# Optimization experiments

Measured on AMD Instinct MI355X. Metric: run time of the kernel, lower is better.

## Reference

```python
import jax, jax.numpy as jnp
from jax import lax
import numpy as np

AE_THRESHOLD = 0.5


def setup_inputs() -> dict:
    key = jax.random.key(0)
    ks = jax.random.split(key, 8)
    B, C, H, W = 8, 80, 128, 128
    return {
        "tl_heat": jax.random.normal(ks[0], (B, C, H, W), jnp.float32),
        "br_heat": jax.random.normal(ks[1], (B, C, H, W), jnp.float32),
        "ct_heat": jax.random.normal(ks[2], (B, C, H, W), jnp.float32),
        "tl_tag": jax.random.normal(ks[3], (B, 1, H, W), jnp.float32),
        "br_tag": jax.random.normal(ks[4], (B, 1, H, W), jnp.float32),
        "tl_regr": jax.random.normal(ks[5], (B, 2, H, W), jnp.float32),
        "br_regr": jax.random.normal(ks[6], (B, 2, H, W), jnp.float32),
        "ct_regr": jax.random.normal(ks[7], (B, 2, H, W), jnp.float32),
        "K": 100,
        "kernel": 3,
        "num_dets": 1000,
    }


def _nms(heat, kernel):
    # maxpool NMS: keep only local maxima (SAME padding, stride 1, NCHW)
    hmax = lax.reduce_window(heat, -jnp.inf, lax.max,
                             (1, 1, kernel, kernel), (1, 1, 1, 1), 'SAME')
    return heat * (hmax == heat).astype(heat.dtype)


def _topk(scores, K):
    B, C, H, W = scores.shape
    s, inds = lax.top_k(scores.reshape(B, -1), K)  # over cat*H*W
    clses = inds // (H * W)
    inds = inds % (H * W)
    ys = (inds // W).astype(jnp.float32)
    xs = (inds % W).astype(jnp.float32)
    return s, inds, clses, ys, xs


def _gather(feat, inds):
    # NCHW -> (B, H*W, C), gather spatial rows by inds (B, K) -> (B, K, C)
    B, C, H, W = feat.shape
    f = feat.transpose(0, 2, 3, 1).reshape(B, H * W, C)
    return jnp.take_along_axis(f, inds[:, :, None], axis=1)


def reference(tl_heat, br_heat, ct_heat, tl_tag, br_tag,
              tl_regr, br_regr, ct_regr, K, kernel, num_dets):
    B, C, H, W = tl_heat.shape

    tl_heat = _nms(jax.nn.sigmoid(tl_heat), kernel)
    br_heat = _nms(jax.nn.sigmoid(br_heat), kernel)
    ct_heat = _nms(jax.nn.sigmoid(ct_heat), kernel)

    tl_s, tl_inds, tl_clses, tl_ys, tl_xs = _topk(tl_heat, K)
    br_s, br_inds, br_clses, br_ys, br_xs = _topk(br_heat, K)
    ct_s, ct_inds, ct_clses, ct_ys, ct_xs = _topk(ct_heat, K)

    tl_off = _gather(tl_regr, tl_inds)  # (B, K, 2)
    br_off = _gather(br_regr, br_inds)
    ct_off = _gather(ct_regr, ct_inds)

    # corner coords with sub-pixel offsets; broadcast to (B, K, K) pairs
    tl_xs_p = (tl_xs + tl_off[..., 0])[:, :, None]  # (B, K, 1)
    tl_ys_p = (tl_ys + tl_off[..., 1])[:, :, None]
    br_xs_p = (br_xs + br_off[..., 0])[:, None, :]  # (B, 1, K)
    br_ys_p = (br_ys + br_off[..., 1])[:, None, :]
    ct_xs_p = ct_xs + ct_off[..., 0]                # (B, K)
    ct_ys_p = ct_ys + ct_off[..., 1]

    pair = (B, K, K)
    bboxes = jnp.stack([jnp.broadcast_to(tl_xs_p, pair),
                        jnp.broadcast_to(tl_ys_p, pair),
                        jnp.broadcast_to(br_xs_p, pair),
                        jnp.broadcast_to(br_ys_p, pair)], axis=-1)  # (B,K,K,4)

    tl_emb = _gather(tl_tag, tl_inds)[:, :, 0]  # (B, K)
    br_emb = _gather(br_tag, br_inds)[:, :, 0]
    dists = jnp.abs(tl_emb[:, :, None] - br_emb[:, None, :])  # (B,K,K)

    scores = (tl_s[:, :, None] + br_s[:, None, :]) * 0.5
    reject = ((tl_clses[:, :, None] != br_clses[:, None, :])
              | (dists > AE_THRESHOLD)
              | (br_xs_p < tl_xs_p)
              | (br_ys_p < tl_ys_p))
    scores = jnp.where(reject, -jnp.ones_like(scores), scores)

    scores, inds = lax.top_k(scores.reshape(B, -1), num_dets)  # (B, num_dets)

    bboxes = jnp.take_along_axis(bboxes.reshape(B, K * K, 4),
                                 inds[:, :, None], axis=1)
    clses_full = jnp.broadcast_to(tl_clses[:, :, None], pair).reshape(B, K * K)
    clses = jnp.take_along_axis(clses_full, inds, axis=1).astype(jnp.float32)
    tl_s_full = jnp.broadcast_to(tl_s[:, :, None], pair).reshape(B, K * K)
    br_s_full = jnp.broadcast_to(br_s[:, None, :], pair).reshape(B, K * K)
    tl_sc = jnp.take_along_axis(tl_s_full, inds, axis=1)
    br_sc = jnp.take_along_axis(br_s_full, inds, axis=1)

    detections = jnp.concatenate([bboxes, scores[..., None], tl_sc[..., None],
                                  br_sc[..., None], clses[..., None]], axis=-1)
    center = jnp.stack([ct_xs_p, ct_ys_p,
                        ct_clses.astype(jnp.float32), ct_s], axis=-1)  # (B,K,4)
    return detections, center
```

## Files before the change

### kernel.cpp

```cpp
#include <hip/hip_runtime.h>
#include <cstdint>

#define NB    8
#define NC    80
#define HH    128
#define WW    128
#define HW    16384
#define CHW   1310720
#define KTOP  100
#define NDET  1000
#define NPAIR 10000
#define CAP   4096
#define ACAP  2048
#define NBINS 4096
#define VTHR  3.5f

#define OFF_CCNT   0
#define OFF_CCNT2  3072
#define OFF_HIST   6144
#define ZERO_BYTES 399360
#define OFF_THR    399360
#define OFF_CAND   399488
#define OFF_CS     1185920
#define OFF_CX     1195520
#define OFF_CY     1205120
#define OFF_CE     1214720
#define OFF_CCLS   1224320
#define WS_NEEDED  1233920

__device__ __forceinline__ float sigmoidf(float x) {
    float e = expf(-fabsf(x));
    return (x >= 0.f ? 1.f : e) / (1.f + e);
}

__global__ void __launch_bounds__(512) k_nms(
        const float* __restrict__ tl, const float* __restrict__ br,
        const float* __restrict__ ct,
        uint64_t* __restrict__ cand, int* __restrict__ ccnt) {
    __shared__ float lds[HW];

    int tid = threadIdx.x;
    int bid = blockIdx.x;
    int bc = bid / NC;
    int chan = bid - bc * NC;
    int t = bc >> 3; int b = bc & 7;
    const float* heat = (t == 0) ? tl : (t == 1) ? br : ct;
    const float* cb = heat + (size_t)b * CHW + (size_t)chan * HW;
    int lane = tid & 63;
    int w = tid >> 6;

    #pragma unroll
    for (int it = 0; it < 8; ++it) {
        int fbase = (it * 8 + w) * 256;
        __builtin_amdgcn_global_load_lds(
            (const __attribute__((address_space(1))) void*)(cb + fbase + lane * 4),
            (__attribute__((address_space(3))) void*)(&lds[fbase]),
            16, 0, 0);
    }
    asm volatile("s_waitcnt vmcnt(0)" ::: "memory");
    __syncthreads();

    int tile_x = (tid & 31) * 4;
    int tile_y = (tid >> 5) * 8;
    const float NEG = -__builtin_inff();
    float4 A, B, C;
    if (tile_y > 0) A = *(const float4*)&lds[(tile_y - 1) * WW + tile_x];
    else            A = make_float4(NEG, NEG, NEG, NEG);
    B = *(const float4*)&lds[tile_y * WW + tile_x];

    int ccbase = bc * 32;
    uint64_t* cd = cand + (size_t)bc * CAP;
    int ibase = chan * HW + tile_y * WW + tile_x;

    #pragma unroll
    for (int j = 0; j < 8; ++j) {
        int yn = tile_y + j + 1;
        if (yn < HH) C = *(const float4*)&lds[yn * WW + tile_x];
        else         C = make_float4(NEG, NEG, NEG, NEG);

        float c0 = fmaxf(fmaxf(A.x, B.x), C.x);
        float c1 = fmaxf(fmaxf(A.y, B.y), C.y);
        float c2 = fmaxf(fmaxf(A.z, B.z), C.z);
        float c3 = fmaxf(fmaxf(A.w, B.w), C.w);
        float cl = __shfl_up(c3, 1);
        float cr = __shfl_down(c0, 1);
        if (tile_x == 0)      cl = NEG;
        if (tile_x == WW - 4) cr = NEG;
        float w0 = fmaxf(fmaxf(cl, c0), c1);
        float w1 = fmaxf(fmaxf(c0, c1), c2);
        float w2 = fmaxf(fmaxf(c1, c2), c3);
        float w3 = fmaxf(fmaxf(c2, c3), cr);

        #define EMIT(Wm, V, P) \
            if ((Wm) == (V) && (V) >= VTHR) { \
                uint32_t bt = __float_as_uint(sigmoidf(V)); \
                int pos = atomicAdd(&ccnt[ccbase], 1); \
                if (pos < CAP) \
                    cd[pos] = ((uint64_t)bt << 32) | \
                              (uint32_t)(~(uint32_t)(ibase + j * WW + (P))); \
            }
        EMIT(w0, B.x, 0)
        EMIT(w1, B.y, 1)
        EMIT(w2, B.z, 2)
        EMIT(w3, B.w, 3)
        #undef EMIT
        A = B; B = C;
    }
}

__device__ uint64_t key_at(const float* __restrict__ hb, int i) {
    float v = hb[i];
    int rem = i & (HW - 1);
    int y = rem >> 7, x = rem & (WW - 1);
    bool mx = true;
    if (y > 0) {
        if (x > 0      && hb[i - WW - 1] > v) mx = false;
        if (              hb[i - WW    ] > v) mx = false;
        if (x < WW - 1 && hb[i - WW + 1] > v) mx = false;
    }
    if (x > 0      && hb[i - 1] > v) mx = false;
    if (x < WW - 1 && hb[i + 1] > v) mx = false;
    if (y < HH - 1) {
        if (x > 0      && hb[i + WW - 1] > v) mx = false;
        if (              hb[i + WW    ] > v) mx = false;
        if (x < WW - 1 && hb[i + WW + 1] > v) mx = false;
    }
    if (!mx) return 0;
    return ((uint64_t)__float_as_uint(sigmoidf(v)) << 32) | (uint32_t)(~(uint32_t)i);
}

__device__ __forceinline__ bool fast_ok(const int* ccnt, int bc) {
    int n = ccnt[bc * 32];
    return (n >= KTOP) && (n <= CAP);
}

__global__ void __launch_bounds__(256) fb_hist(
        const int* __restrict__ ccnt,
        const float* __restrict__ tl, const float* __restrict__ br,
        const float* __restrict__ ct, uint32_t* __restrict__ hist) {
    int bc = blockIdx.y;
    if (fast_ok(ccnt, bc)) return;
    __shared__ uint32_t lh[NBINS];
    for (int i = threadIdx.x; i < NBINS; i += 256) lh[i] = 0;
    __syncthreads();
    int t = bc >> 3; int b = bc & 7;
    const float* heat = (t == 0) ? tl : (t == 1) ? br : ct;
    const float* hb = heat + (size_t)b * CHW;
    for (int i = blockIdx.x * 256 + threadIdx.x; i < CHW; i += 32 * 256) {
        uint64_t k = key_at(hb, i);
        if (k) atomicAdd(&lh[(uint32_t)(k >> 51)], 1u);
    }
    __syncthreads();
    uint32_t* gh = hist + (size_t)bc * NBINS;
    for (int i = threadIdx.x; i < NBINS; i += 256) {
        uint32_t c = lh[i];
        if (c) atomicAdd(&gh[i], c);
    }
}

__global__ void __launch_bounds__(256) fb_thresh(
        const int* __restrict__ ccnt, const uint32_t* __restrict__ hist,
        int* __restrict__ thr) {
    int bc = blockIdx.x;
    if (fast_ok(ccnt, bc)) return;
    __shared__ uint32_t csum[256];
    const uint32_t* h = hist + (size_t)bc * NBINS;
    int tid = threadIdx.x;
    uint32_t bins[16];
    #pragma unroll
    for (int i = 0; i < 16; ++i) bins[i] = h[tid * 16 + i];
    if (tid == 0) bins[0] = 0;
    uint32_t s = 0;
    #pragma unroll
    for (int i = 0; i < 16; ++i) s += bins[i];
    csum[tid] = s;
    __syncthreads();
    for (int step = 1; step < 256; step <<= 1) {
        uint32_t add = (tid + step < 256) ? csum[tid + step] : 0;
        __syncthreads();
        csum[tid] += add;
        __syncthreads();
    }
    uint32_t inc = csum[tid];
    uint32_t above = (tid + 1 < 256) ? csum[tid + 1] : 0;
    if (tid == 0 && inc < KTOP) thr[bc] = 1;
    if (above < KTOP && inc >= KTOP) {
        uint32_t cum = above;
        int T = 1;
        #pragma unroll
        for (int i = 15; i >= 0; --i) {
            cum += bins[i];
            if (cum >= KTOP) { T = tid * 16 + i; break; }
        }
        thr[bc] = T;
    }
}

__global__ void __launch_bounds__(256) fb_collect(
        const int* __restrict__ ccnt, const int* __restrict__ thr,
        const float* __restrict__ tl, const float* __restrict__ br,
        const float* __restrict__ ct,
        uint64_t* __restrict__ cand, int* __restrict__ ccnt2) {
    int bc = blockIdx.y;
    if (fast_ok(ccnt, bc)) return;
    int t = bc >> 3; int b = bc & 7;
    const float* heat = (t == 0) ? tl : (t == 1) ? br : ct;
    const float* hb = heat + (size_t)b * CHW;
    int T = thr[bc];
    for (int i = blockIdx.x * 256 + threadIdx.x; i < CHW; i += 32 * 256) {
        uint64_t k = key_at(hb, i);
        if (k && (int)(uint32_t)(k >> 51) >= T) {
            int pc = atomicAdd(&ccnt2[bc * 32], 1);
            if (pc < CAP) cand[(size_t)bc * CAP + pc] = k;
        }
    }
}

template <int N>
__device__ void bitonic_desc(uint64_t* k) {
    for (int kk = 2; kk <= N; kk <<= 1) {
        for (int j = kk >> 1; j > 0; j >>= 1) {
            __syncthreads();
            for (int i = threadIdx.x; i < N; i += blockDim.x) {
                int l = i ^ j;
                if (l > i) {
                    uint64_t a = k[i], b = k[l];
                    bool up = ((i & kk) == 0);
                    if (up ? (a < b) : (a > b)) { k[i] = b; k[l] = a; }
                }
            }
        }
    }
    __syncthreads();
}

__global__ void __launch_bounds__(1024) k_select(
        const uint64_t* __restrict__ cand, const int* __restrict__ ccnt,
        const int* __restrict__ ccnt2,
        const float* __restrict__ tl_tag, const float* __restrict__ br_tag,
        const float* __restrict__ tl_regr, const float* __restrict__ br_regr,
        const float* __restrict__ ct_regr,
        float* __restrict__ cs, float* __restrict__ cx, float* __restrict__ cy,
        float* __restrict__ ce, int* __restrict__ ccls) {
    __shared__ uint64_t keys[CAP];
    int bc = blockIdx.x; int t = bc >> 3; int b = bc & 7;
    int nf = ccnt[bc * 32];
    bool ok = (nf >= KTOP) && (nf <= CAP);
    int n = ok ? nf : ccnt2[bc * 32];
    if (n > CAP) n = CAP;
    if (n <= 512) {
        for (int i = threadIdx.x; i < 512; i += 1024)
            keys[i] = (i < n) ? cand[(size_t)bc * CAP + i] : 0ull;
        bitonic_desc<512>(keys);
    } else if (n <= 2048) {
        for (int i = threadIdx.x; i < 2048; i += 1024)
            keys[i] = (i < n) ? cand[(size_t)bc * CAP + i] : 0ull;
        bitonic_desc<2048>(keys);
    } else {
        for (int i = threadIdx.x; i < CAP; i += 1024)
            keys[i] = (i < n) ? cand[(size_t)bc * CAP + i] : 0ull;
        bitonic_desc<CAP>(keys);
    }
    if (threadIdx.x < KTOP) {
        uint64_t key = keys[threadIdx.x];
        float s = __uint_as_float((uint32_t)(key >> 32));
        uint32_t idx = ~(uint32_t)key;
        int cls = (int)(idx >> 14);
        int rem = (int)(idx & (HW - 1));
        int y = rem >> 7, x = rem & (WW - 1);
        const float* regr = (t == 0) ? tl_regr : (t == 1) ? br_regr : ct_regr;
        float o0 = regr[((size_t)b * 2 + 0) * HW + rem];
        float o1 = regr[((size_t)b * 2 + 1) * HW + rem];
        float emb = 0.f;
        if (t == 0) emb = tl_tag[(size_t)b * HW + rem];
        else if (t == 1) emb = br_tag[(size_t)b * HW + rem];
        int o = bc * KTOP + threadIdx.x;
        cs[o] = s;
        cx[o] = (float)x + o0;
        cy[o] = (float)y + o1;
        ce[o] = emb;
        ccls[o] = cls;
    }
}

__global__ void __launch_bounds__(1024) k_pairfinal(
        const float* __restrict__ cs, const float* __restrict__ cx,
        const float* __restrict__ cy, const float* __restrict__ ce,
        const int* __restrict__ ccls, float* __restrict__ out) {
    int b = blockIdx.x;
    __shared__ float ts[KTOP], tx[KTOP], ty[KTOP], te[KTOP];
    __shared__ int   tc[KTOP];
    __shared__ float bs_[KTOP], bx[KTOP], by[KTOP], be[KTOP];
    __shared__ int   bcl[KTOP];
    __shared__ uint64_t acc[ACAP];
    __shared__ int aidx[ACAP];
    __shared__ int acnt_s;
    int tid = threadIdx.x;
    if (tid == 0) acnt_s = 0;
    if (tid < KTOP) {
        int o = (0 * NB + b) * KTOP + tid;
        ts[tid] = cs[o]; tx[tid] = cx[o]; ty[tid] = cy[o]; te[tid] = ce[o]; tc[tid] = ccls[o];
    } else if (tid >= 512 && tid < 512 + KTOP) {
        int k = tid - 512;
        int o = (1 * NB + b) * KTOP + k;
        bs_[k] = cs[o]; bx[k] = cx[o]; by[k] = cy[o]; be[k] = ce[o]; bcl[k] = ccls[o];
    }
    __syncthreads();
    for (int p = tid; p < NPAIR; p += 1024) {
        int i = p / KTOP, j = p - i * KTOP;
        bool rej = (tc[i] != bcl[j])
                 | (fabsf(te[i] - be[j]) > 0.5f)
                 | (bx[j] < tx[i])
                 | (by[j] < ty[i]);
        if (!rej) {
            float sc = (ts[i] + bs_[j]) * 0.5f;
            int pos = atomicAdd(&acnt_s, 1);
            if (pos < ACAP)
                acc[pos] = ((uint64_t)__float_as_uint(sc) << 32) | (uint32_t)(~(uint32_t)p);
        }
    }
    __syncthreads();
    int m = acnt_s; if (m > ACAP) m = ACAP;
    if (m <= 256) {
        for (int i = tid; i < 256; i += 1024) if (i >= m) acc[i] = 0;
        bitonic_desc<256>(acc);
    } else {
        for (int i = tid; i < ACAP; i += 1024) if (i >= m) acc[i] = 0;
        bitonic_desc<ACAP>(acc);
    }
    for (int i = tid; i < m; i += 1024) aidx[i] = (int)(~(uint32_t)acc[i]);
    __syncthreads();
    for (int d = tid; d < NDET; d += 1024) {
        int p; float sc;
        if (d < m) {
            p = aidx[d];
            sc = __uint_as_float((uint32_t)(acc[d] >> 32));
        } else {
            int r = d - m;
            int idx = r;
            for (;;) {
                int c = 0;
                for (int a = 0; a < m; ++a) c += (aidx[a] <= idx) ? 1 : 0;
                int ni = r + c;
                if (ni == idx) break;
                idx = ni;
            }
            p = idx; sc = -1.f;
        }
        int i = p / KTOP, j = p - i * KTOP;
        int ot = (0 * NB + b) * KTOP + i;
        int ob = (1 * NB + b) * KTOP + j;
        float* dr = out + ((size_t)b * NDET + d) * 8;
        dr[0] = cx[ot]; dr[1] = cy[ot]; dr[2] = cx[ob]; dr[3] = cy[ob];
        dr[4] = sc; dr[5] = cs[ot]; dr[6] = cs[ob]; dr[7] = (float)ccls[ot];
    }
    if (tid < KTOP) {
        int oc = (2 * NB + b) * KTOP + tid;
        float* cr = out + (size_t)NB * NDET * 8 + ((size_t)b * KTOP + tid) * 4;
        cr[0] = cx[oc]; cr[1] = cy[oc]; cr[2] = (float)ccls[oc]; cr[3] = cs[oc];
    }
}

extern "C" void kernel_launch(void* const* d_in, const int* in_sizes, int n_in,
                              void* d_out, int out_size, void* d_ws, size_t ws_size,
                              hipStream_t stream) {
    const float* tl_heat = (const float*)d_in[0];
    const float* br_heat = (const float*)d_in[1];
    const float* ct_heat = (const float*)d_in[2];
    const float* tl_tag  = (const float*)d_in[3];
    const float* br_tag  = (const float*)d_in[4];
    const float* tl_regr = (const float*)d_in[5];
    const float* br_regr = (const float*)d_in[6];
    const float* ct_regr = (const float*)d_in[7];

    if (ws_size < (size_t)WS_NEEDED) return;

    char* ws = (char*)d_ws;
    int*      ccnt  = (int*)(ws + OFF_CCNT);
    int*      ccnt2 = (int*)(ws + OFF_CCNT2);
    uint32_t* hist  = (uint32_t*)(ws + OFF_HIST);
    int*      thr   = (int*)(ws + OFF_THR);
    uint64_t* cand  = (uint64_t*)(ws + OFF_CAND);
    float*    cs    = (float*)(ws + OFF_CS);
    float*    cx    = (float*)(ws + OFF_CX);
    float*    cy    = (float*)(ws + OFF_CY);
    float*    ce    = (float*)(ws + OFF_CE);
    int*      ccls  = (int*)(ws + OFF_CCLS);

    hipMemsetAsync(ws, 0, ZERO_BYTES, stream);

    k_nms<<<24 * NC, 512, 0, stream>>>(tl_heat, br_heat, ct_heat, cand, ccnt);
    fb_hist<<<dim3(32, 24), 256, 0, stream>>>(ccnt, tl_heat, br_heat, ct_heat, hist);
    fb_thresh<<<24, 256, 0, stream>>>(ccnt, hist, thr);
    fb_collect<<<dim3(32, 24), 256, 0, stream>>>(ccnt, thr,
                                                 tl_heat, br_heat, ct_heat,
                                                 cand, ccnt2);
    k_select<<<24, 1024, 0, stream>>>(cand, ccnt, ccnt2, tl_tag, br_tag,
                                      tl_regr, br_regr, ct_regr,
                                      cs, cx, cy, ce, ccls);
    k_pairfinal<<<NB, 1024, 0, stream>>>(cs, cx, cy, ce, ccls, (float*)d_out);
}
```

Before: 68.08 us.

## Split NMS per channel into four row-strip blocks with halo rows

The NMS kernel now launches four blocks per (tensor, batch, channel), each staging a 32-row strip plus two halo rows into a smaller LDS buffer through plain float4 loads. This replaces the single 512-thread block that staged the whole 128x128 plane with async global_load_lds. The intent is to raise occupancy, since each block needs much less LDS, and to spread the work over more blocks. In exchange it loads halo rows twice and gives up the direct-to-LDS load path.

```diff
diff --git a/kernel.cpp b/kernel.cpp
--- a/kernel.cpp
+++ b/kernel.cpp
@@ -33,51 +33,48 @@
     return (x >= 0.f ? 1.f : e) / (1.f + e);
 }
 
-__global__ void __launch_bounds__(512) k_nms(
+__global__ void __launch_bounds__(256) k_nms(
         const float* __restrict__ tl, const float* __restrict__ br,
         const float* __restrict__ ct,
         uint64_t* __restrict__ cand, int* __restrict__ ccnt) {
-    __shared__ float lds[HW];
+    __shared__ float lds[34 * WW];
 
     int tid = threadIdx.x;
     int bid = blockIdx.x;
-    int bc = bid / NC;
-    int chan = bid - bc * NC;
+    int bc = bid >> 8;
+    bc = bid / 320;
+    int rem_b = bid - bc * 320;
+    int chan = rem_b >> 2;
+    int q = rem_b & 3;
     int t = bc >> 3; int b = bc & 7;
     const float* heat = (t == 0) ? tl : (t == 1) ? br : ct;
     const float* cb = heat + (size_t)b * CHW + (size_t)chan * HW;
-    int lane = tid & 63;
-    int w = tid >> 6;
-
-    #pragma unroll
-    for (int it = 0; it < 8; ++it) {
-        int fbase = (it * 8 + w) * 256;
-        __builtin_amdgcn_global_load_lds(
-            (const __attribute__((address_space(1))) void*)(cb + fbase + lane * 4),
-            (__attribute__((address_space(3))) void*)(&lds[fbase]),
-            16, 0, 0);
-    }
-    asm volatile("s_waitcnt vmcnt(0)" ::: "memory");
-    __syncthreads();
-
-    int tile_x = (tid & 31) * 4;
-    int tile_y = (tid >> 5) * 8;
+    int ybase = q * 32;
     const float NEG = -__builtin_inff();
-    float4 A, B, C;
-    if (tile_y > 0) A = *(const float4*)&lds[(tile_y - 1) * WW + tile_x];
-    else            A = make_float4(NEG, NEG, NEG, NEG);
-    B = *(const float4*)&lds[tile_y * WW + tile_x];
-
+
+    for (int k = tid; k < 34 * 32; k += 256) {
+        int r = k >> 5;
+        int c4 = (k & 31) << 2;
+        int gy = ybase - 1 + r;
+        int gyc = min(max(gy, 0), HH - 1);
+        float4 v = *(const float4*)(cb + gyc * WW + c4);
+        if (gy < 0 || gy > HH - 1) v = make_float4(NEG, NEG, NEG, NEG);
+        *(float4*)&lds[r * WW + c4] = v;
+    }
+    __syncthreads();
+
+    int rg = tid >> 5;
+    int tile_x = (tid & 31) << 2;
+    int lrow = 1 + rg * 4;
+    float4 A = *(const float4*)&lds[(lrow - 1) * WW + tile_x];
+    float4 B = *(const float4*)&lds[lrow * WW + tile_x];
     int ccbase = bc * 32;
     uint64_t* cd = cand + (size_t)bc * CAP;
-    int ibase = chan * HW + tile_y * WW + tile_x;
+    int ibase = chan * HW + (ybase + rg * 4) * WW + tile_x;
 
     #pragma unroll
-    for (int j = 0; j < 8; ++j) {
-        int yn = tile_y + j + 1;
-        if (yn < HH) C = *(const float4*)&lds[yn * WW + tile_x];
-        else         C = make_float4(NEG, NEG, NEG, NEG);
-
+    for (int j = 0; j < 4; ++j) {
+        float4 C = *(const float4*)&lds[(lrow + j + 1) * WW + tile_x];
         float c0 = fmaxf(fmaxf(A.x, B.x), C.x);
         float c1 = fmaxf(fmaxf(A.y, B.y), C.y);
         float c2 = fmaxf(fmaxf(A.z, B.z), C.z);
@@ -389,7 +386,7 @@
 
     hipMemsetAsync(ws, 0, ZERO_BYTES, stream);
 
-    k_nms<<<24 * NC, 512, 0, stream>>>(tl_heat, br_heat, ct_heat, cand, ccnt);
+    k_nms<<<24 * NC * 4, 256, 0, stream>>>(tl_heat, br_heat, ct_heat, cand, ccnt);
     fb_hist<<<dim3(32, 24), 256, 0, stream>>>(ccnt, tl_heat, br_heat, ct_heat, hist);
     fb_thresh<<<24, 256, 0, stream>>>(ccnt, hist, thr);
     fb_collect<<<dim3(32, 24), 256, 0, stream>>>(ccnt, thr,
```

Measured after the change: 65.26 us. -4.1%, faster.
